# Performance work log

Hardware: AMD Instinct MI355X
Metric: run time of the kernel (lower is better)

The kernel has to match this reference:

```python
import jax, jax.numpy as jnp
import numpy as np

NUM_MOL = 1024
KE = 14.399645351950548
KEHALF = KE / 2.0
CUTOFF = 10.0  # PhysNetCutOff(10.0)


def physnet_cutoff(d):
    # PhysNet smooth cutoff: 1 - 6u^5 + 15u^4 - 10u^3 for d < rc, else 0
    u = d / CUTOFF
    fc = 1.0 - 6.0 * u**5 + 15.0 * u**4 - 10.0 * u**3
    return jnp.where(d < CUTOFF, fc, 0.0)


def setup_inputs() -> dict:
    key = jax.random.key(0)
    k = jax.random.split(key, 5)
    N, E = 100000, 3200000
    # atomic numbers as floats in [1, 94]
    Z = jax.random.randint(k[0], (N,), 1, 95).astype(jnp.float32)
    # pair displacement vectors; norm ~ O(3) Angstrom, well inside cutoff
    r_ij = jax.random.normal(k[1], (E, 3), dtype=jnp.float32) * 2.0
    idx_i = jax.random.randint(k[2], (E,), 0, N, dtype=jnp.int32)
    idx_j = jax.random.randint(k[3], (E,), 0, N, dtype=jnp.int32)
    # per-atom molecule index, sorted (maxm = idx_m[-1] + 1 in the original)
    idx_m = jnp.sort(jax.random.randint(k[4], (N,), 0, NUM_MOL, dtype=jnp.int32))
    adiv = jnp.ones((1,), jnp.float32)
    apow = jnp.ones((1,), jnp.float32)
    a_vector = jnp.ones((4,), jnp.float32)
    c_vector = jnp.ones((4,), jnp.float32)
    return dict(Z=Z, r_ij=r_ij, idx_i=idx_i, idx_j=idx_j, idx_m=idx_m,
                adiv=adiv, apow=apow, a_vector=a_vector, c_vector=c_vector)


def reference(Z, r_ij, idx_i, idx_j, idx_m, adiv, apow, a_vector, c_vector):
    N = Z.shape[0]
    d = jnp.linalg.norm(r_ij, axis=1)                      # (E,)
    cut = physnet_cutoff(d)                                # (E,)
    z = Z ** jax.nn.softplus(apow[0])                      # (N,)
    a = (z[idx_i] + z[idx_j]) * jax.nn.softplus(adiv[0])   # (E,)
    a_comp = jax.nn.softplus(a_vector)[:, None] * a        # (4, E)
    c = jax.nn.softplus(c_vector)
    c_normed = c / jnp.sum(jnp.abs(c))                     # L1-normalize over dim 0
    f_temp = jnp.einsum('k,ke->e', c_normed, jnp.exp(-a_comp * d))  # (E,)
    f = f_temp * cut
    zizj = Z[idx_i] * Z[idx_j]
    e_edge = KEHALF * f * zizj / d                          # (E,)
    y_atom = jax.ops.segment_sum(e_edge, idx_i, num_segments=N)        # (N,)
    y = jax.ops.segment_sum(y_atom, idx_m, num_segments=NUM_MOL)       # (NUM_MOL,)
    return y
```

## Files before the change

kernel.cpp:

```cpp
#include <hip/hip_runtime.h>
#include <hip/hip_bf16.h>

#define NUM_MOL 1024
#define KEHALF 7.199822675975274f
#define RCUT 10.0f

__device__ __forceinline__ float softplus_f(float x) {
    return (x > 20.0f) ? x : log1pf(__expf(x));
}

__global__ void zbl_prep_kernel(const float* __restrict__ Z,
                                const int* __restrict__ idx_m,
                                const float* __restrict__ apow,
                                float4* __restrict__ atab, int N) {
    int n = blockIdx.x * blockDim.x + threadIdx.x;
    if (n >= N) return;
    float p = softplus_f(apow[0]);
    float z = Z[n];
    float zp = __powf(z, p);
    atab[n] = make_float4(z, zp, __int_as_float(idx_m[n]), 0.0f);
}

__global__ __launch_bounds__(256) void zbl_edge_kernel(
    const float* __restrict__ r_ij,
    const int* __restrict__ idx_i,
    const int* __restrict__ idx_j,
    const float4* __restrict__ atab,
    const float* __restrict__ adiv,
    const float* __restrict__ a_vector,
    const float* __restrict__ c_vector,
    float* __restrict__ y, int E)
{
    __shared__ float bins[NUM_MOL];
    for (int b = threadIdx.x; b < NUM_MOL; b += blockDim.x) bins[b] = 0.0f;
    __syncthreads();

    const float sp_adiv = softplus_f(adiv[0]);
    const float sa0 = softplus_f(a_vector[0]);
    const float sa1 = softplus_f(a_vector[1]);
    const float sa2 = softplus_f(a_vector[2]);
    const float sa3 = softplus_f(a_vector[3]);
    float c0 = softplus_f(c_vector[0]);
    float c1 = softplus_f(c_vector[1]);
    float c2 = softplus_f(c_vector[2]);
    float c3 = softplus_f(c_vector[3]);
    const float cs = fabsf(c0) + fabsf(c1) + fabsf(c2) + fabsf(c3);
    const float cinv = 1.0f / cs;
    c0 *= cinv; c1 *= cinv; c2 *= cinv; c3 *= cinv;

    const int stride = gridDim.x * blockDim.x;
    for (int e = blockIdx.x * blockDim.x + threadIdx.x; e < E; e += stride) {
        const int i = idx_i[e];
        const int j = idx_j[e];
        const float4 ai = atab[i];
        const float4 aj = atab[j];
        const float x  = r_ij[3 * e + 0];
        const float yy = r_ij[3 * e + 1];
        const float zz = r_ij[3 * e + 2];
        const float d = sqrtf(x * x + yy * yy + zz * zz);

        const float u = d * (1.0f / RCUT);
        const float u3 = u * u * u;
        float fc = 1.0f + u3 * (-10.0f + u * (15.0f - 6.0f * u));
        fc = (d < RCUT) ? fc : 0.0f;

        const float a = (ai.y + aj.y) * sp_adiv;
        const float ad = a * d;
        const float ft = c0 * __expf(-sa0 * ad) + c1 * __expf(-sa1 * ad)
                       + c2 * __expf(-sa2 * ad) + c3 * __expf(-sa3 * ad);

        const float ee = KEHALF * ft * fc * ai.x * aj.x / d;
        atomicAdd(&bins[__float_as_int(ai.z)], ee);
    }

    __syncthreads();
    for (int b = threadIdx.x; b < NUM_MOL; b += blockDim.x) {
        const float v = bins[b];
        if (v != 0.0f) atomicAdd(&y[b], v);
    }
}

__global__ __launch_bounds__(256) void zbl_edge_kernel_nows(
    const float* __restrict__ r_ij,
    const int* __restrict__ idx_i,
    const int* __restrict__ idx_j,
    const float* __restrict__ Z,
    const int* __restrict__ idx_m,
    const float* __restrict__ adiv,
    const float* __restrict__ apow,
    const float* __restrict__ a_vector,
    const float* __restrict__ c_vector,
    float* __restrict__ y, int E)
{
    __shared__ float bins[NUM_MOL];
    for (int b = threadIdx.x; b < NUM_MOL; b += blockDim.x) bins[b] = 0.0f;
    __syncthreads();

    const float sp_apow = softplus_f(apow[0]);
    const float sp_adiv = softplus_f(adiv[0]);
    const float sa0 = softplus_f(a_vector[0]);
    const float sa1 = softplus_f(a_vector[1]);
    const float sa2 = softplus_f(a_vector[2]);
    const float sa3 = softplus_f(a_vector[3]);
    float c0 = softplus_f(c_vector[0]);
    float c1 = softplus_f(c_vector[1]);
    float c2 = softplus_f(c_vector[2]);
    float c3 = softplus_f(c_vector[3]);
    const float cs = fabsf(c0) + fabsf(c1) + fabsf(c2) + fabsf(c3);
    const float cinv = 1.0f / cs;
    c0 *= cinv; c1 *= cinv; c2 *= cinv; c3 *= cinv;

    const int stride = gridDim.x * blockDim.x;
    for (int e = blockIdx.x * blockDim.x + threadIdx.x; e < E; e += stride) {
        const int i = idx_i[e];
        const int j = idx_j[e];
        const float zi = Z[i];
        const float zj = Z[j];
        const float x  = r_ij[3 * e + 0];
        const float yy = r_ij[3 * e + 1];
        const float zz = r_ij[3 * e + 2];
        const float d = sqrtf(x * x + yy * yy + zz * zz);

        const float u = d * (1.0f / RCUT);
        const float u3 = u * u * u;
        float fc = 1.0f + u3 * (-10.0f + u * (15.0f - 6.0f * u));
        fc = (d < RCUT) ? fc : 0.0f;

        const float a = (__powf(zi, sp_apow) + __powf(zj, sp_apow)) * sp_adiv;
        const float ad = a * d;
        const float ft = c0 * __expf(-sa0 * ad) + c1 * __expf(-sa1 * ad)
                       + c2 * __expf(-sa2 * ad) + c3 * __expf(-sa3 * ad);

        const float ee = KEHALF * ft * fc * zi * zj / d;
        atomicAdd(&bins[idx_m[i]], ee);
    }

    __syncthreads();
    for (int b = threadIdx.x; b < NUM_MOL; b += blockDim.x) {
        const float v = bins[b];
        if (v != 0.0f) atomicAdd(&y[b], v);
    }
}

extern "C" void kernel_launch(void* const* d_in, const int* in_sizes, int n_in,
                              void* d_out, int out_size, void* d_ws, size_t ws_size,
                              hipStream_t stream) {
    const float* Z        = (const float*)d_in[0];
    const float* r_ij     = (const float*)d_in[1];
    const int*   idx_i    = (const int*)d_in[2];
    const int*   idx_j    = (const int*)d_in[3];
    const int*   idx_m    = (const int*)d_in[4];
    const float* adiv     = (const float*)d_in[5];
    const float* apow     = (const float*)d_in[6];
    const float* a_vector = (const float*)d_in[7];
    const float* c_vector = (const float*)d_in[8];
    float* y = (float*)d_out;

    const int N = in_sizes[0];
    const int E = in_sizes[1] / 3;

    hipMemsetAsync(y, 0, (size_t)out_size * sizeof(float), stream);

    const size_t atab_bytes = (size_t)N * sizeof(float4);
    if (ws_size >= atab_bytes) {
        float4* atab = (float4*)d_ws;
        zbl_prep_kernel<<<(N + 255) / 256, 256, 0, stream>>>(Z, idx_m, apow, atab, N);
        zbl_edge_kernel<<<1024, 256, 0, stream>>>(r_ij, idx_i, idx_j, atab,
                                                  adiv, a_vector, c_vector, y, E);
    } else {
        zbl_edge_kernel_nows<<<1024, 256, 0, stream>>>(r_ij, idx_i, idx_j, Z, idx_m,
                                                       adiv, apow, a_vector, c_vector, y, E);
    }
}
```

Before: 137.7 us.

## Vectorize edge loads four-per-thread, use rsqrt, and rotate global bin flush

The edge kernel now processes four edges per thread using int4 index loads and three float4 loads of r_ij, which issues all eight atom-table gathers up front to raise memory-level parallelism. It replaces sqrt and divide with rsqrt, makes the uniform coefficients scalar via readfirstlane, and skips zero-valued shared atomics. Block size grows to 512, and each block's flush of its bins to global memory starts at a block-dependent offset to reduce contention on the same addresses. The vector loads assume 16-byte alignment of the inputs, and register pressure rises with four edges in flight.

```diff
diff --git a/kernel.cpp b/kernel.cpp
--- a/kernel.cpp
+++ b/kernel.cpp
@@ -1,12 +1,15 @@
 #include <hip/hip_runtime.h>
-#include <hip/hip_bf16.h>
 
 #define NUM_MOL 1024
 #define KEHALF 7.199822675975274f
 #define RCUT 10.0f
 
 __device__ __forceinline__ float softplus_f(float x) {
-    return (x > 20.0f) ? x : log1pf(__expf(x));
+    return (x > 20.0f) ? x : __logf(1.0f + __expf(x));
+}
+
+__device__ __forceinline__ float uni(float x) {
+    return __int_as_float(__builtin_amdgcn_readfirstlane(__float_as_int(x)));
 }
 
 __global__ void zbl_prep_kernel(const float* __restrict__ Z,
@@ -21,10 +24,13 @@
     atab[n] = make_float4(z, zp, __int_as_float(idx_m[n]), 0.0f);
 }
 
-__global__ __launch_bounds__(256) void zbl_edge_kernel(
-    const float* __restrict__ r_ij,
+__global__ __launch_bounds__(512) void zbl_edge_kernel(
+    const float4* __restrict__ r4,
+    const int4* __restrict__ idx_i4,
+    const int4* __restrict__ idx_j4,
     const int* __restrict__ idx_i,
     const int* __restrict__ idx_j,
+    const float* __restrict__ r_ij,
     const float4* __restrict__ atab,
     const float* __restrict__ adiv,
     const float* __restrict__ a_vector,
@@ -35,46 +41,79 @@
     for (int b = threadIdx.x; b < NUM_MOL; b += blockDim.x) bins[b] = 0.0f;
     __syncthreads();
 
-    const float sp_adiv = softplus_f(adiv[0]);
-    const float sa0 = softplus_f(a_vector[0]);
-    const float sa1 = softplus_f(a_vector[1]);
-    const float sa2 = softplus_f(a_vector[2]);
-    const float sa3 = softplus_f(a_vector[3]);
+    const float sp_adiv = uni(softplus_f(adiv[0]));
+    const float sa0 = uni(softplus_f(a_vector[0]));
+    const float sa1 = uni(softplus_f(a_vector[1]));
+    const float sa2 = uni(softplus_f(a_vector[2]));
+    const float sa3 = uni(softplus_f(a_vector[3]));
     float c0 = softplus_f(c_vector[0]);
     float c1 = softplus_f(c_vector[1]);
     float c2 = softplus_f(c_vector[2]);
     float c3 = softplus_f(c_vector[3]);
-    const float cs = fabsf(c0) + fabsf(c1) + fabsf(c2) + fabsf(c3);
-    const float cinv = 1.0f / cs;
-    c0 *= cinv; c1 *= cinv; c2 *= cinv; c3 *= cinv;
-
-    const int stride = gridDim.x * blockDim.x;
-    for (int e = blockIdx.x * blockDim.x + threadIdx.x; e < E; e += stride) {
-        const int i = idx_i[e];
-        const int j = idx_j[e];
-        const float4 ai = atab[i];
-        const float4 aj = atab[j];
-        const float x  = r_ij[3 * e + 0];
-        const float yy = r_ij[3 * e + 1];
-        const float zz = r_ij[3 * e + 2];
-        const float d = sqrtf(x * x + yy * yy + zz * zz);
-
+    const float cinv = 1.0f / (fabsf(c0) + fabsf(c1) + fabsf(c2) + fabsf(c3));
+    const float k0 = uni(c0 * cinv);
+    const float k1 = uni(c1 * cinv);
+    const float k2 = uni(c2 * cinv);
+    const float k3 = uni(c3 * cinv);
+
+    auto edge = [&](const float4& ai, const float4& aj, float d2) {
+        const float rinv = rsqrtf(d2);
+        const float d = d2 * rinv;
         const float u = d * (1.0f / RCUT);
         const float u3 = u * u * u;
         float fc = 1.0f + u3 * (-10.0f + u * (15.0f - 6.0f * u));
         fc = (d < RCUT) ? fc : 0.0f;
-
         const float a = (ai.y + aj.y) * sp_adiv;
         const float ad = a * d;
-        const float ft = c0 * __expf(-sa0 * ad) + c1 * __expf(-sa1 * ad)
-                       + c2 * __expf(-sa2 * ad) + c3 * __expf(-sa3 * ad);
-
-        const float ee = KEHALF * ft * fc * ai.x * aj.x / d;
-        atomicAdd(&bins[__float_as_int(ai.z)], ee);
-    }
-
-    __syncthreads();
-    for (int b = threadIdx.x; b < NUM_MOL; b += blockDim.x) {
+        const float ft = k0 * __expf(-sa0 * ad) + k1 * __expf(-sa1 * ad)
+                       + k2 * __expf(-sa2 * ad) + k3 * __expf(-sa3 * ad);
+        const float ee = KEHALF * ft * fc * ai.x * aj.x * rinv;
+        if (ee != 0.0f) atomicAdd(&bins[__float_as_int(ai.z)], ee);
+    };
+
+    const int t = blockIdx.x * blockDim.x + threadIdx.x;
+    const int nthr = gridDim.x * blockDim.x;
+    const int E4 = E >> 2;
+
+    for (int g = t; g < E4; g += nthr) {
+        const int4 vi = idx_i4[g];
+        const int4 vj = idx_j4[g];
+        const float4 ai0 = atab[vi.x];
+        const float4 ai1 = atab[vi.y];
+        const float4 ai2 = atab[vi.z];
+        const float4 ai3 = atab[vi.w];
+        const float4 aj0 = atab[vj.x];
+        const float4 aj1 = atab[vj.y];
+        const float4 aj2 = atab[vj.z];
+        const float4 aj3 = atab[vj.w];
+        const float4 r0 = r4[3 * g + 0];
+        const float4 r1 = r4[3 * g + 1];
+        const float4 r2 = r4[3 * g + 2];
+
+        const float d2_0 = r0.x * r0.x + r0.y * r0.y + r0.z * r0.z;
+        const float d2_1 = r0.w * r0.w + r1.x * r1.x + r1.y * r1.y;
+        const float d2_2 = r1.z * r1.z + r1.w * r1.w + r2.x * r2.x;
+        const float d2_3 = r2.y * r2.y + r2.z * r2.z + r2.w * r2.w;
+
+        edge(ai0, aj0, d2_0);
+        edge(ai1, aj1, d2_1);
+        edge(ai2, aj2, d2_2);
+        edge(ai3, aj3, d2_3);
+    }
+
+    for (int e = (E4 << 2) + t; e < E; e += nthr) {
+        const float4 ai = atab[idx_i[e]];
+        const float4 aj = atab[idx_j[e]];
+        const float x  = r_ij[3 * e + 0];
+        const float yy = r_ij[3 * e + 1];
+        const float zz = r_ij[3 * e + 2];
+        edge(ai, aj, x * x + yy * yy + zz * zz);
+    }
+
+    __syncthreads();
+    const int rot = (blockIdx.x << 3) & (NUM_MOL - 1);
+    for (int k = threadIdx.x; k < NUM_MOL; k += blockDim.x) {
+        const int b = (k + rot) & (NUM_MOL - 1);
         const float v = bins[b];
         if (v != 0.0f) atomicAdd(&y[b], v);
     }
@@ -165,10 +204,11 @@
     if (ws_size >= atab_bytes) {
         float4* atab = (float4*)d_ws;
         zbl_prep_kernel<<<(N + 255) / 256, 256, 0, stream>>>(Z, idx_m, apow, atab, N);
-        zbl_edge_kernel<<<1024, 256, 0, stream>>>(r_ij, idx_i, idx_j, atab,
-                                                  adiv, a_vector, c_vector, y, E);
+        zbl_edge_kernel<<<1024, 512, 0, stream>>>(
+            (const float4*)r_ij, (const int4*)idx_i, (const int4*)idx_j,
+            idx_i, idx_j, r_ij, atab, adiv, a_vector, c_vector, y, E);
     } else {
-        zbl_edge_kernel_nows<<<1024, 256, 0, stream>>>(r_ij, idx_i, idx_j, Z, idx_m,
+        zbl_edge_kernel_nows<<<2048, 256, 0, stream>>>(r_ij, idx_i, idx_j, Z, idx_m,
                                                        adiv, apow, a_vector, c_vector, y, E);
     }
 }
```

Measured after the change: 139.0 us. Within noise of the previous version (+1.0%).
